# Kernel tuning notes

Hardware: AMD Instinct MI355X
Metric: run time of the kernel (lower is better)

The kernel has to match this reference:

```python
import jax, jax.numpy as jnp
import numpy as np
from jax import lax

RENDER_SIZE = (228, 304)   # (H, W) from __init__ default
FAR = 100.0                # z-buffer init, matches depth_map fill in source
EPS = 1e-7
CHUNK = 128                # faces processed per scan step


def setup_inputs() -> dict:
    key = jax.random.key(0)
    k1, k2, k3 = jax.random.split(key, 3)
    B, N, M = 1, 8192, 2048
    H, W = RENDER_SIZE
    uv = jax.random.uniform(k1, (B, N, 2), dtype=jnp.float32)           # u,v in [0,1]
    d = jax.random.uniform(k2, (B, N, 1), dtype=jnp.float32) * 4.0 + 1.0  # depth in [1,5]
    verts = jnp.concatenate([uv, d], axis=-1)                            # [B,N,3] depthmap format
    faces = jax.random.randint(k3, (B, M, 3), 0, N)                      # [B,M,3]
    fx = fy = 260.0
    K = jnp.array([[fx, 0.0, W / 2.0], [0.0, fy, H / 2.0], [0.0, 0.0, 1.0]], jnp.float32)
    intrinsics = jnp.tile(K[None], (B, 1, 1))
    ang = 0.02  # small camera rotation about y
    R = jnp.array([[np.cos(ang), 0.0, np.sin(ang)], [0.0, 1.0, 0.0],
                   [-np.sin(ang), 0.0, np.cos(ang)]], jnp.float32)
    R_mat = jnp.tile(R[None], (B, 1, 1))
    t_mat = jnp.tile(jnp.array([[0.01], [0.0], [0.02]], jnp.float32)[None], (B, 1, 1))
    return {"verts": verts, "faces": faces, "intrinsics": intrinsics,
            "R_mat": R_mat, "t_mat": t_mat}


def _convert_depthmap_to_cam(verts, K, H, W):
    # depthmap (u,v,d) -> camera coords; mirrors convert_depthmap_to_cam
    d = verts[..., 2:3]
    pix = jnp.concatenate([verts[..., 0:1] * W, verts[..., 1:2] * H,
                           jnp.ones_like(d)], axis=-1)                   # [B,N,3]
    Kinv = jnp.linalg.inv(K)
    return jnp.einsum('bij,bnj->bni', Kinv, pix) * d


def _project_cam_to_depthmap(cam, K, H, W):
    # camera coords -> depthmap (u,v,z); mirrors project_cam_to_depthmap
    z = cam[..., 2]
    p = jnp.stack([cam[..., 0] / (z + EPS), cam[..., 1] / (z + EPS),
                   jnp.ones_like(z)], axis=-1)
    p = jnp.einsum('bnj,bij->bni', p, K)  # matmul(p, K^T)
    u = jnp.clip(p[..., 0] / W, 0.0, 1.0)
    v = jnp.clip(p[..., 1] / H, 0.0, 1.0)
    return jnp.stack([u, v, z], axis=-1)


def _transform_depthmap(verts, K, R, t, H, W):
    cam = _convert_depthmap_to_cam(verts, K, H, W)                       # [B,N,3]
    cam2 = jnp.einsum('bij,bnj->bni', R, cam) + t[:, :, 0][:, None, :]   # R@x + t
    return _project_cam_to_depthmap(cam2, K, H, W)


def _rasterize(face_verts, S):
    """face_verts: [B,M,3,3] NDC (x,y) + depth z. Returns depth [B,S,S], sil [B,S,S]."""
    B, M = face_verts.shape[0], face_verts.shape[1]
    p = (2.0 * jnp.arange(S, dtype=face_verts.dtype) + 1.0 - S) / S      # NR pixel centers
    XP = p[None, None, None, :]   # x varies along last axis
    YP = p[None, None, :, None]   # y varies along rows

    chunks = face_verts.reshape(B, M // CHUNK, CHUNK, 3, 3).transpose(1, 0, 2, 3, 4)

    def step(carry, fvc):  # fvc: [B,C,3,3]
        depth, sil = carry
        x = fvc[..., 0][..., None, None]  # [B,C,3,1,1]
        y = fvc[..., 1][..., None, None]
        z = fvc[..., 2][..., None, None]
        x0, x1, x2 = x[:, :, 0], x[:, :, 1], x[:, :, 2]
        y0, y1, y2 = y[:, :, 0], y[:, :, 1], y[:, :, 2]
        z0, z1, z2 = z[:, :, 0], z[:, :, 1], z[:, :, 2]
        denom = (y1 - y2) * (x0 - x2) + (x2 - x1) * (y0 - y2)
        ok = jnp.abs(denom) > 1e-10
        safe = jnp.where(ok, denom, 1.0)
        w0 = ((y1 - y2) * (XP - x2) + (x2 - x1) * (YP - y2)) / safe      # [B,C,S,S]
        w1 = ((y2 - y0) * (XP - x2) + (x0 - x2) * (YP - y2)) / safe
        w2 = 1.0 - w0 - w1
        inside = (w0 >= 0) & (w1 >= 0) & (w2 >= 0) & ok
        inv_z = w0 / z0 + w1 / z1 + w2 / z2  # perspective-correct depth interp
        zp = 1.0 / jnp.where(jnp.abs(inv_z) > EPS, inv_z, EPS)
        zc = jnp.where(inside & (zp > 0), zp, FAR)
        depth = jnp.minimum(depth, zc.min(axis=1))                       # z-buffer update
        sil = jnp.maximum(sil, inside.any(axis=1).astype(depth.dtype))
        return (depth, sil), None

    init = (jnp.full((B, S, S), FAR, face_verts.dtype),
            jnp.zeros((B, S, S), face_verts.dtype))
    (depth, sil), _ = lax.scan(step, init, chunks)
    return depth, sil


def reference(verts, faces, intrinsics, R_mat, t_mat):
    H, W = RENDER_SIZE
    S = max(H, W)
    v = _transform_depthmap(verts, intrinsics, R_mat, t_mat, H, W)       # reprojected depthmap
    # depthmap [0,1] -> NDC [-1,1], keeping aspect via img_max_size
    ndc = jnp.concatenate([v[:, :, :1] * W / S * 2.0 - 1.0,
                           v[:, :, 1:2] * H / S * 2.0 - 1.0,
                           v[:, :, 2:]], axis=2)
    fv = jax.vmap(lambda vb, fb: vb[fb])(ndc, faces)                     # [B,M,3,3]
    depth, sil = _rasterize(fv, S)
    depth = depth[:, ::-1, :][:, :H, :W]  # flip(dim=1) then crop, as in _render
    sil = sil[:, ::-1, :][:, :H, :W]
    return jnp.stack([depth, sil], axis=1)  # [B,2,H,W]: depth + silhouette
```

## Files before the change

kernel.cpp:

```cpp
#include <hip/hip_runtime.h>

#define SS 304
#define HH 228
#define WW 304
#define FARV 100.0f
#define EPSV 1e-07f
#define SPLIT 16
#define CH 128
#define TILE 32

__device__ __forceinline__ void xform_vertex(
    float u, float v, float d,
    float fx, float cx, float fy, float cy,
    float r00, float r01, float r02,
    float r10, float r11, float r12,
    float r20, float r21, float r22,
    float t0, float t1, float t2,
    float& xn, float& yn, float& z)
{
#pragma clang fp contract(off)
    float ki00 = 1.0f / fx;
    float ki02 = -(cx / fx);
    float ki11 = 1.0f / fy;
    float ki12 = -(cy / fy);
    float px = u * (float)WW;
    float py = v * (float)HH;
    float c0 = (ki00 * px + ki02) * d;
    float c1 = (ki11 * py + ki12) * d;
    float c2 = d;
    float e0 = ((r00*c0 + r01*c1) + r02*c2) + t0;
    float e1 = ((r10*c0 + r11*c1) + r12*c2) + t1;
    float e2 = ((r20*c0 + r21*c1) + r22*c2) + t2;
    z = e2;
    float zd = z + EPSV;
    float p0 = e0 / zd;
    float p1 = e1 / zd;
    float q0 = p0 * fx + cx;
    float q1 = p1 * fy + cy;
    float uu = q0 / (float)WW; uu = fminf(fmaxf(uu, 0.0f), 1.0f);
    float vv = q1 / (float)HH; vv = fminf(fmaxf(vv, 0.0f), 1.0f);
    xn = uu * (float)WW / (float)SS * 2.0f - 1.0f;
    yn = vv * (float)HH / (float)SS * 2.0f - 1.0f;
}

__global__ __launch_bounds__(256) void prep_kernel(
    const float* __restrict__ verts,
    const int* __restrict__ faces,
    const float* __restrict__ Km,
    const float* __restrict__ Rm,
    const float* __restrict__ tm,
    float4* __restrict__ bboxArr,
    float4* __restrict__ P0arr,
    float4* __restrict__ P1arr,
    float*  __restrict__ Garr,
    float* __restrict__ out, int M)
{
#pragma clang fp contract(off)
    int g = blockIdx.x * blockDim.x + threadIdx.x;
    if (g < HH * WW) {
        out[g] = FARV;
        out[HH * WW + g] = 0.0f;
    }
    if (g >= M) return;
    int m = g;
    int i0 = faces[3*m+0], i1 = faces[3*m+1], i2 = faces[3*m+2];
    float fx = Km[0], cx = Km[2], fy = Km[4], cy = Km[5];
    float r00 = Rm[0], r01 = Rm[1], r02 = Rm[2];
    float r10 = Rm[3], r11 = Rm[4], r12 = Rm[5];
    float r20 = Rm[6], r21 = Rm[7], r22 = Rm[8];
    float t0 = tm[0], t1 = tm[1], t2 = tm[2];

    float x0, y0, z0, x1, y1, z1, x2, y2, z2;
    xform_vertex(verts[3*i0+0], verts[3*i0+1], verts[3*i0+2], fx,cx,fy,cy,
                 r00,r01,r02,r10,r11,r12,r20,r21,r22,t0,t1,t2, x0,y0,z0);
    xform_vertex(verts[3*i1+0], verts[3*i1+1], verts[3*i1+2], fx,cx,fy,cy,
                 r00,r01,r02,r10,r11,r12,r20,r21,r22,t0,t1,t2, x1,y1,z1);
    xform_vertex(verts[3*i2+0], verts[3*i2+1], verts[3*i2+2], fx,cx,fy,cy,
                 r00,r01,r02,r10,r11,r12,r20,r21,r22,t0,t1,t2, x2,y2,z2);

    float A0 = y1 - y2;
    float B0 = x2 - x1;
    float A1 = y2 - y0;
    float B1 = x0 - x2;
    float dy02 = y0 - y2;
    float denom = A0 * B1 + B0 * dy02;
    bool ok = fabsf(denom) > 1e-10f;

    float xmin, xmax, ymin, ymax;
    if (ok) {
        xmin = fminf(x0, fminf(x1, x2)) - 1e-4f;
        xmax = fmaxf(x0, fmaxf(x1, x2)) + 1e-4f;
        ymin = fminf(y0, fminf(y1, y2)) - 1e-4f;
        ymax = fmaxf(y0, fmaxf(y1, y2)) + 1e-4f;
    } else {
        xmin = 1e30f; xmax = -1e30f; ymin = 1e30f; ymax = -1e30f;
    }
    bboxArr[m] = make_float4(xmin, xmax, ymin, ymax);

    float rs = 1.0f / denom;
    float a0 = A0 * rs, b0 = B0 * rs;
    float c0 = -(a0 * x2 + b0 * y2);
    float a1 = A1 * rs, b1 = B1 * rs;
    float c1 = -(a1 * x2 + b1 * y2);
    float rz0 = 1.0f / z0, rz1 = 1.0f / z1, rz2 = 1.0f / z2;
    float u = rz0 - rz2, v = rz1 - rz2;
    float E = a0 * u + a1 * v;
    float F = b0 * u + b1 * v;
    float G = (c0 * u + c1 * v) + rz2;

    P0arr[m] = make_float4(a0, b0, c0, a1);
    P1arr[m] = make_float4(b1, c1, E, F);
    Garr[m]  = G;
}

__global__ __launch_bounds__(128) void raster_kernel(
    const float4* __restrict__ bboxArr,
    const float4* __restrict__ P0arr,
    const float4* __restrict__ P1arr,
    const float*  __restrict__ Garr,
    float* __restrict__ out, int M)
{
    __shared__ float4 sP0[CH];
    __shared__ float4 sP1[CH];
    __shared__ float  sG[CH];
    __shared__ int sCount;

    int tx = threadIdx.x;
    int ty = threadIdx.y;
    int tid = ty * 16 + tx;

    int wbase = blockIdx.x * TILE;
    int hbase = blockIdx.y * TILE;

    int whi = min(wbase + TILE - 1, WW - 1);
    int hhi = min(hbase + TILE - 1, HH - 1);
    float txlo = ((float)(2*wbase + 1 - SS)) / (float)SS;
    float txhi = ((float)(2*whi   + 1 - SS)) / (float)SS;
    float tylo = ((float)(2*(SS-1-hhi)   + 1 - SS)) / (float)SS;
    float tyhi = ((float)(2*(SS-1-hbase) + 1 - SS)) / (float)SS;

    if (tid == 0) sCount = 0;
    __syncthreads();

    {
        int m = blockIdx.z * CH + tid;
        float4 rb = bboxArr[m];
        bool pass = !(rb.x > txhi || rb.y < txlo || rb.z > tyhi || rb.w < tylo);
        if (pass) {
            int i = atomicAdd(&sCount, 1);
            sP0[i] = P0arr[m];
            sP1[i] = P1arr[m];
            sG[i]  = Garr[m];
        }
    }
    __syncthreads();
    int cnt = sCount;

    int w0px = wbase + 2 * tx;
    int h0px = hbase + 4 * ty;
    float XP0 = ((float)(2*w0px + 1 - SS)) / (float)SS;
    float YP0 = ((float)(SS - 1 - 2*h0px)) / (float)SS;
    const float dx = 2.0f / (float)SS;
    const float dy = -2.0f / (float)SS;

    float mx[4][2] = {{0,0},{0,0},{0,0},{0,0}};

    for (int k = 0; k < cnt; ++k) {
        float4 g0 = sP0[k];
        float4 g1 = sP1[k];
        float  G  = sG[k];
        float a0 = g0.x, b0 = g0.y, c0 = g0.z, a1 = g0.w;
        float b1 = g1.x, c1 = g1.y, E = g1.z, F = g1.w;

        float p0 = fmaf(a0, XP0, fmaf(b0, YP0, c0));
        float p1 = fmaf(a1, XP0, fmaf(b1, YP0, c1));
        float pz = fmaf(E,  XP0, fmaf(F,  YP0, G));
        float a0dx = a0 * dx, a1dx = a1 * dx, Edx = E * dx;
        float b0dy = b0 * dy, b1dy = b1 * dy, Fdy = F * dy;

#pragma unroll
        for (int yy = 0; yy < 4; ++yy) {
            float w2 = (1.0f - p0) - p1;
            float m3 = fminf(fminf(p0, p1), w2);
            mx[yy][0] = fmaxf(mx[yy][0], (m3 >= 0.0f) ? pz : 0.0f);
            float q0 = p0 + a0dx;
            float q1 = p1 + a1dx;
            float qz = pz + Edx;
            float w2r = (1.0f - q0) - q1;
            float m3r = fminf(fminf(q0, q1), w2r);
            mx[yy][1] = fmaxf(mx[yy][1], (m3r >= 0.0f) ? qz : 0.0f);
            p0 += b0dy; p1 += b1dy; pz += Fdy;
        }
    }

#pragma unroll
    for (int yy = 0; yy < 4; ++yy) {
        int h = h0px + yy;
        if (h >= HH) break;
#pragma unroll
        for (int xx = 0; xx < 2; ++xx) {
            int w = w0px + xx;
            if (w >= WW) continue;
            float m = mx[yy][xx];
            if (m > 0.0f) {
                float depth = __builtin_amdgcn_rcpf(m);
                atomicMin((unsigned int*)&out[h * WW + w], __float_as_uint(depth));
                atomicMax((unsigned int*)&out[HH * WW + h * WW + w],
                          __float_as_uint(1.0f));
            }
        }
    }
}

extern "C" void kernel_launch(void* const* d_in, const int* in_sizes, int n_in,
                              void* d_out, int out_size, void* d_ws, size_t ws_size,
                              hipStream_t stream) {
    const float* verts = (const float*)d_in[0];
    const int*   faces = (const int*)d_in[1];
    const float* K     = (const float*)d_in[2];
    const float* R     = (const float*)d_in[3];
    const float* t     = (const float*)d_in[4];
    float* out = (float*)d_out;

    int M = in_sizes[1] / 3;

    char* ws = (char*)d_ws;
    float4* bbox = (float4*)ws;                ws += (size_t)M * sizeof(float4);
    float4* P0   = (float4*)ws;                ws += (size_t)M * sizeof(float4);
    float4* P1   = (float4*)ws;                ws += (size_t)M * sizeof(float4);
    float*  G    = (float*)ws;                 ws += (size_t)M * sizeof(float);

    prep_kernel<<<(HH * WW + 255) / 256, 256, 0, stream>>>(
        verts, faces, K, R, t, bbox, P0, P1, G, out, M);

    dim3 blk(16, 8);
    dim3 grd((WW + TILE - 1) / TILE, (HH + TILE - 1) / TILE, SPLIT);
    raster_kernel<<<grd, blk, 0, stream>>>(bbox, P0, P1, G, out, M);
}
```

Before: 91.88 us.

## Replace atomic z-buffer with per-split slices and a merge kernel, smaller tiles

The rasterizer now uses 16x16 pixel tiles with 64-thread blocks, 8 face splits of 256 faces each, and 2x2 pixels per thread. Each split writes its per-pixel max inverse depth to its own slice buffer, so global atomicMin/atomicMax are no longer needed. A new merge kernel reduces across the slices and writes depth and silhouette, which also takes over output initialisation from the prep kernel. This adds a third launch and extra global traffic for the slices, in exchange for more blocks, finer bbox culling per tile and no atomics.

```diff
diff --git a/kernel.cpp b/kernel.cpp
--- a/kernel.cpp
+++ b/kernel.cpp
@@ -3,11 +3,12 @@
 #define SS 304
 #define HH 228
 #define WW 304
+#define HPW (HH * WW)
 #define FARV 100.0f
 #define EPSV 1e-07f
-#define SPLIT 16
-#define CH 128
-#define TILE 32
+#define SPLIT 8
+#define CH 256
+#define TILE 16
 
 __device__ __forceinline__ void xform_vertex(
     float u, float v, float d,
@@ -53,16 +54,11 @@
     float4* __restrict__ P0arr,
     float4* __restrict__ P1arr,
     float*  __restrict__ Garr,
-    float* __restrict__ out, int M)
+    int M)
 {
 #pragma clang fp contract(off)
-    int g = blockIdx.x * blockDim.x + threadIdx.x;
-    if (g < HH * WW) {
-        out[g] = FARV;
-        out[HH * WW + g] = 0.0f;
-    }
-    if (g >= M) return;
-    int m = g;
+    int m = blockIdx.x * blockDim.x + threadIdx.x;
+    if (m >= M) return;
     int i0 = faces[3*m+0], i1 = faces[3*m+1], i2 = faces[3*m+2];
     float fx = Km[0], cx = Km[2], fy = Km[4], cy = Km[5];
     float r00 = Rm[0], r01 = Rm[1], r02 = Rm[2];
@@ -103,22 +99,22 @@
     float a1 = A1 * rs, b1 = B1 * rs;
     float c1 = -(a1 * x2 + b1 * y2);
     float rz0 = 1.0f / z0, rz1 = 1.0f / z1, rz2 = 1.0f / z2;
-    float u = rz0 - rz2, v = rz1 - rz2;
-    float E = a0 * u + a1 * v;
-    float F = b0 * u + b1 * v;
-    float G = (c0 * u + c1 * v) + rz2;
+    float uu = rz0 - rz2, vv = rz1 - rz2;
+    float E = a0 * uu + a1 * vv;
+    float F = b0 * uu + b1 * vv;
+    float G = (c0 * uu + c1 * vv) + rz2;
 
     P0arr[m] = make_float4(a0, b0, c0, a1);
     P1arr[m] = make_float4(b1, c1, E, F);
     Garr[m]  = G;
 }
 
-__global__ __launch_bounds__(128) void raster_kernel(
+__global__ __launch_bounds__(64) void raster_kernel(
     const float4* __restrict__ bboxArr,
     const float4* __restrict__ P0arr,
     const float4* __restrict__ P1arr,
     const float*  __restrict__ Garr,
-    float* __restrict__ out, int M)
+    float* __restrict__ slice)
 {
     __shared__ float4 sP0[CH];
     __shared__ float4 sP1[CH];
@@ -127,7 +123,7 @@
 
     int tx = threadIdx.x;
     int ty = threadIdx.y;
-    int tid = ty * 16 + tx;
+    int tid = ty * 8 + tx;
 
     int wbase = blockIdx.x * TILE;
     int hbase = blockIdx.y * TILE;
@@ -142,8 +138,9 @@
     if (tid == 0) sCount = 0;
     __syncthreads();
 
-    {
-        int m = blockIdx.z * CH + tid;
+#pragma unroll
+    for (int j = 0; j < CH / 64; ++j) {
+        int m = blockIdx.z * CH + j * 64 + tid;
         float4 rb = bboxArr[m];
         bool pass = !(rb.x > txhi || rb.y < txlo || rb.z > tyhi || rb.w < tylo);
         if (pass) {
@@ -157,13 +154,13 @@
     int cnt = sCount;
 
     int w0px = wbase + 2 * tx;
-    int h0px = hbase + 4 * ty;
+    int h0px = hbase + 2 * ty;
     float XP0 = ((float)(2*w0px + 1 - SS)) / (float)SS;
     float YP0 = ((float)(SS - 1 - 2*h0px)) / (float)SS;
-    const float dx = 2.0f / (float)SS;
-    const float dy = -2.0f / (float)SS;
-
-    float mx[4][2] = {{0,0},{0,0},{0,0},{0,0}};
+    const float dxx = 2.0f / (float)SS;
+    const float dyy = -2.0f / (float)SS;
+
+    float m00 = 0.0f, m10 = 0.0f, m01 = 0.0f, m11 = 0.0f;
 
     for (int k = 0; k < cnt; ++k) {
         float4 g0 = sP0[k];
@@ -175,41 +172,53 @@
         float p0 = fmaf(a0, XP0, fmaf(b0, YP0, c0));
         float p1 = fmaf(a1, XP0, fmaf(b1, YP0, c1));
         float pz = fmaf(E,  XP0, fmaf(F,  YP0, G));
-        float a0dx = a0 * dx, a1dx = a1 * dx, Edx = E * dx;
-        float b0dy = b0 * dy, b1dy = b1 * dy, Fdy = F * dy;
-
+        float a0x = a0 * dxx, a1x = a1 * dxx, Ex = E * dxx;
+        float b0y = b0 * dyy, b1y = b1 * dyy, Fy = F * dyy;
+
+        float w2 = (1.0f - p0) - p1;
+        float m3 = fminf(fminf(p0, p1), w2);
+        m00 = fmaxf(m00, (m3 >= 0.0f) ? pz : 0.0f);
+        float q0 = p0 + a0x, q1 = p1 + a1x, qz = pz + Ex;
+        float w2b = (1.0f - q0) - q1;
+        float m3b = fminf(fminf(q0, q1), w2b);
+        m10 = fmaxf(m10, (m3b >= 0.0f) ? qz : 0.0f);
+        float r0 = p0 + b0y, r1 = p1 + b1y, rz = pz + Fy;
+        float w2c = (1.0f - r0) - r1;
+        float m3c = fminf(fminf(r0, r1), w2c);
+        m01 = fmaxf(m01, (m3c >= 0.0f) ? rz : 0.0f);
+        float s0 = q0 + b0y, s1 = q1 + b1y, sz = qz + Fy;
+        float w2d = (1.0f - s0) - s1;
+        float m3d = fminf(fminf(s0, s1), w2d);
+        m11 = fmaxf(m11, (m3d >= 0.0f) ? sz : 0.0f);
+    }
+
+    float* sb = slice + (size_t)blockIdx.z * HPW;
+    if (h0px < HH) {
+        float2 v = make_float2(m00, m10);
+        *(float2*)&sb[h0px * WW + w0px] = v;
+    }
+    if (h0px + 1 < HH) {
+        float2 v = make_float2(m01, m11);
+        *(float2*)&sb[(h0px + 1) * WW + w0px] = v;
+    }
+}
+
+__global__ __launch_bounds__(256) void merge_kernel(
+    const float* __restrict__ slice, float* __restrict__ out)
+{
+    int i = blockIdx.x * blockDim.x + threadIdx.x;
+    if (i >= HPW) return;
+    float mx = slice[i];
 #pragma unroll
-        for (int yy = 0; yy < 4; ++yy) {
-            float w2 = (1.0f - p0) - p1;
-            float m3 = fminf(fminf(p0, p1), w2);
-            mx[yy][0] = fmaxf(mx[yy][0], (m3 >= 0.0f) ? pz : 0.0f);
-            float q0 = p0 + a0dx;
-            float q1 = p1 + a1dx;
-            float qz = pz + Edx;
-            float w2r = (1.0f - q0) - q1;
-            float m3r = fminf(fminf(q0, q1), w2r);
-            mx[yy][1] = fmaxf(mx[yy][1], (m3r >= 0.0f) ? qz : 0.0f);
-            p0 += b0dy; p1 += b1dy; pz += Fdy;
-        }
-    }
-
-#pragma unroll
-    for (int yy = 0; yy < 4; ++yy) {
-        int h = h0px + yy;
-        if (h >= HH) break;
-#pragma unroll
-        for (int xx = 0; xx < 2; ++xx) {
-            int w = w0px + xx;
-            if (w >= WW) continue;
-            float m = mx[yy][xx];
-            if (m > 0.0f) {
-                float depth = __builtin_amdgcn_rcpf(m);
-                atomicMin((unsigned int*)&out[h * WW + w], __float_as_uint(depth));
-                atomicMax((unsigned int*)&out[HH * WW + h * WW + w],
-                          __float_as_uint(1.0f));
-            }
-        }
-    }
+    for (int s = 1; s < SPLIT; ++s)
+        mx = fmaxf(mx, slice[(size_t)s * HPW + i]);
+    float depth = FARV, sil = 0.0f;
+    if (mx > 0.0f) {
+        depth = __builtin_amdgcn_rcpf(mx);
+        sil = 1.0f;
+    }
+    out[i] = depth;
+    out[HPW + i] = sil;
 }
 
 extern "C" void kernel_launch(void* const* d_in, const int* in_sizes, int n_in,
@@ -229,11 +238,14 @@
     float4* P0   = (float4*)ws;                ws += (size_t)M * sizeof(float4);
     float4* P1   = (float4*)ws;                ws += (size_t)M * sizeof(float4);
     float*  G    = (float*)ws;                 ws += (size_t)M * sizeof(float);
-
-    prep_kernel<<<(HH * WW + 255) / 256, 256, 0, stream>>>(
-        verts, faces, K, R, t, bbox, P0, P1, G, out, M);
-
-    dim3 blk(16, 8);
+    float*  slice= (float*)ws;                 ws += (size_t)SPLIT * HPW * sizeof(float);
+
+    prep_kernel<<<(M + 255) / 256, 256, 0, stream>>>(
+        verts, faces, K, R, t, bbox, P0, P1, G, M);
+
+    dim3 blk(8, 8);
     dim3 grd((WW + TILE - 1) / TILE, (HH + TILE - 1) / TILE, SPLIT);
-    raster_kernel<<<grd, blk, 0, stream>>>(bbox, P0, P1, G, out, M);
-}
+    raster_kernel<<<grd, blk, 0, stream>>>(bbox, P0, P1, G, slice);
+
+    merge_kernel<<<(HPW + 255) / 256, 256, 0, stream>>>(slice, out);
+}
```

Result: no change. 90.35 us (-1.7%).
